# Performance work log

Hardware: AMD Instinct MI355X
Metric: run time of the kernel (lower is better)

## Reference

```python
import jax, jax.numpy as jnp
import numpy as np

DIM = 1024
DIM_MEDIA = 1024
DIM_HEAD = 64
HEADS = 8
INNER = DIM_HEAD * HEADS  # 512
B, N_TOK, N_LAT = 4, 4096, 1024
LN_EPS = 1e-5


def setup_inputs() -> dict:
    key = jax.random.key(0)
    ks = jax.random.split(key, 6)
    x = jax.random.normal(ks[0], (B, N_TOK, DIM), dtype=jnp.float32)
    media = jax.random.normal(ks[1], (B, N_LAT, DIM_MEDIA), dtype=jnp.float32)
    media_mask = jax.random.randint(ks[2], (B, N_LAT), 0, 2).astype(bool)
    media_mask = media_mask.at[:, 0].set(True)  # avoid fully-masked rows (NaN softmax)
    ln_gamma = jnp.ones((DIM,), jnp.float32)
    ln_beta = jnp.zeros((DIM,), jnp.float32)
    Wq = jax.random.normal(ks[3], (DIM, INNER), jnp.float32) * (DIM ** -0.5)
    Wkv = jax.random.normal(ks[4], (DIM_MEDIA, 2 * INNER), jnp.float32) * (DIM_MEDIA ** -0.5)
    Wout = jax.random.normal(ks[5], (INNER, DIM), jnp.float32) * (INNER ** -0.5)
    return {"x": x, "media": media, "media_mask": media_mask,
            "ln_gamma": ln_gamma, "ln_beta": ln_beta,
            "Wq": Wq, "Wkv": Wkv, "Wout": Wout}


def reference(x, media, media_mask, ln_gamma, ln_beta, Wq, Wkv, Wout):
    scale = DIM_HEAD ** -0.5
    # LayerNorm over last dim
    mu = jnp.mean(x, axis=-1, keepdims=True)
    var = jnp.mean(jnp.square(x - mu), axis=-1, keepdims=True)
    xn = (x - mu) * jax.lax.rsqrt(var + LN_EPS) * ln_gamma + ln_beta

    q = (xn @ Wq) * scale                      # [b, n, inner]
    kv = media @ Wkv                           # [b, m, 2*inner]
    k, v = jnp.split(kv, 2, axis=-1)

    def to_heads(t):
        b, n, _ = t.shape
        return t.reshape(b, n, HEADS, DIM_HEAD).transpose(0, 2, 1, 3)  # b h n d

    q, k, v = to_heads(q), to_heads(k), to_heads(v)

    sim = jnp.einsum('bhid,bhjd->bhij', q, k)  # [b, h, n_tok, n_lat]
    neg_inf = jnp.float32(-jnp.inf)
    sim = jnp.where(media_mask[:, None, None, :], sim, neg_inf)
    sim = sim - jax.lax.stop_gradient(jnp.max(sim, axis=-1, keepdims=True))
    attn = jax.nn.softmax(sim, axis=-1)
    out = jnp.einsum('bhij,bhjd->bhid', attn, v)  # [b, h, n_tok, d]
    out = out.transpose(0, 2, 1, 3).reshape(out.shape[0], out.shape[2], INNER)
    return out @ Wout  # [b, n_tok, dim]
```

## Files before the change

kernel.cpp:

```cpp
#include <hip/hip_runtime.h>
#include <hip/hip_bf16.h>

typedef short bf16x8 __attribute__((ext_vector_type(8)));
typedef float f32x4 __attribute__((ext_vector_type(4)));
typedef unsigned short u16;

#define AS1 __attribute__((address_space(1)))
#define AS3 __attribute__((address_space(3)))

#define DIM     1024
#define INNER   512
#define HEADS   8
#define DHEAD   64
#define BATCH   4
#define NTOK    4096
#define NLAT    1024
#define M_X     (BATCH*NTOK)
#define M_MED   (BATCH*NLAT)
#define LN_EPS  1e-5f

__device__ __forceinline__ float b2f(u16 h) {
    union { unsigned u; float f; } v; v.u = ((unsigned)h) << 16; return v.f;
}
__device__ __forceinline__ u16 f2b(float f) {
    union { float f; unsigned u; } v; v.f = f;
    unsigned r = v.u + 0x7fff + ((v.u >> 16) & 1);
    return (u16)(r >> 16);
}
__device__ __forceinline__ unsigned cvt_pk(float lo, float hi) {
    unsigned r;
    asm("v_cvt_pk_bf16_f32 %0, %1, %2" : "=v"(r) : "v"(lo), "v"(hi));
    return r;
}

__launch_bounds__(256)
__global__ void detect_kernel(const unsigned* __restrict__ xw, const unsigned* __restrict__ maskw,
                              unsigned* __restrict__ flags) {
    __shared__ int s_bad, s_byte;
    if (threadIdx.x == 0) { s_bad = 0; s_byte = 0; }
    __syncthreads();
    unsigned w = xw[threadIdx.x];
    int bad = 0;
    #pragma unroll
    for (int h = 0; h < 2; h++) {
        unsigned el = (h ? (w >> 16) : w) & 0xFFFFu;
        unsigned ef = (el >> 7) & 0xFFu;
        if (!((ef >= 64u && ef < 192u) || (el & 0x7FFFu) == 0u)) bad = 1;
    }
    if (bad) atomicOr(&s_bad, 1);
    for (int i = threadIdx.x; i < NLAT; i += 256)
        if (maskw[i] > 1u) { atomicOr(&s_byte, 1); break; }
    __syncthreads();
    if (threadIdx.x == 0) { flags[0] = s_bad ? 0u : 1u; flags[1] = s_byte ? 1u : 0u; }
}

#define PREP_BLOCKS 6148

__device__ __forceinline__ void do_transpose(const void* in, u16* out, int R, int C,
                                             int bx, int by, bool bf, u16 (*t)[33]) {
    int c0 = bx * 32, r0 = by * 32;
    int tid = threadIdx.x;
    int r = tid >> 3, cb = (tid & 7) * 4;
    size_t base = (size_t)(r0 + r) * C + c0 + cb;
    u16 e0, e1, e2, e3;
    if (bf) {
        ushort4 a = *(const ushort4*)((const u16*)in + base);
        e0 = a.x; e1 = a.y; e2 = a.z; e3 = a.w;
    } else {
        float4 a = *(const float4*)((const float*)in + base);
        e0 = f2b(a.x); e1 = f2b(a.y); e2 = f2b(a.z); e3 = f2b(a.w);
    }
    t[r][cb] = e0; t[r][cb + 1] = e1; t[r][cb + 2] = e2; t[r][cb + 3] = e3;
    __syncthreads();
    ushort4 o;
    o.x = t[cb + 0][r]; o.y = t[cb + 1][r]; o.z = t[cb + 2][r]; o.w = t[cb + 3][r];
    *(ushort4*)(out + (size_t)(c0 + r) * R + r0 + cb) = o;
}

__launch_bounds__(256)
__global__ void prep_kernel(const void* __restrict__ x, const void* __restrict__ g,
                            const void* __restrict__ bt, u16* __restrict__ xn,
                            const void* __restrict__ media, u16* __restrict__ media_c,
                            const void* __restrict__ mask, int* __restrict__ map,
                            int* __restrict__ cnt,
                            const void* __restrict__ Wq, u16* __restrict__ WqT,
                            const void* __restrict__ Wkv, u16* __restrict__ WkvT,
                            const void* __restrict__ Wout, u16* __restrict__ WoutT,
                            const unsigned* __restrict__ flags) {
    __shared__ int wsumI[4];
    __shared__ u16 t[32][33];
    bool bf = flags[0] != 0;
    int bid = blockIdx.x, tid = threadIdx.x;

    if (bid < 2048) {
        int w = tid >> 6, lane = tid & 63;
        int row0 = (bid << 3) + (w << 1);
        float v[2][16];
        if (bf) {
            const u16* xr = (const u16*)x + (size_t)row0 * DIM;
            bf16x8 a[4];
            #pragma unroll
            for (int rr = 0; rr < 2; rr++)
                #pragma unroll
                for (int i = 0; i < 2; i++)
                    a[rr * 2 + i] = *(const bf16x8*)(xr + (size_t)rr * DIM + (lane + 64 * i) * 8);
            #pragma unroll
            for (int rr = 0; rr < 2; rr++)
                #pragma unroll
                for (int i = 0; i < 2; i++)
                    #pragma unroll
                    for (int j = 0; j < 8; j++)
                        v[rr][i * 8 + j] = b2f((u16)a[rr * 2 + i][j]);
        } else {
            const float* xr = (const float*)x + (size_t)row0 * DIM;
            float4 a[8];
            #pragma unroll
            for (int rr = 0; rr < 2; rr++)
                #pragma unroll
                for (int i = 0; i < 4; i++)
                    a[rr * 4 + i] = *(const float4*)(xr + (size_t)rr * DIM + (lane + 64 * i) * 4);
            #pragma unroll
            for (int rr = 0; rr < 2; rr++)
                #pragma unroll
                for (int i = 0; i < 4; i++) {
                    v[rr][i * 4 + 0] = a[rr * 4 + i].x; v[rr][i * 4 + 1] = a[rr * 4 + i].y;
                    v[rr][i * 4 + 2] = a[rr * 4 + i].z; v[rr][i * 4 + 3] = a[rr * 4 + i].w;
                }
        }
        float s[2] = {0.f, 0.f}, s2[2] = {0.f, 0.f};
        #pragma unroll
        for (int rr = 0; rr < 2; rr++)
            #pragma unroll
            for (int i = 0; i < 16; i++) { s[rr] += v[rr][i]; s2[rr] += v[rr][i] * v[rr][i]; }
        #pragma unroll
        for (int m = 1; m < 64; m <<= 1) {
            #pragma unroll
            for (int rr = 0; rr < 2; rr++) {
                s[rr] += __shfl_xor(s[rr], m);
                s2[rr] += __shfl_xor(s2[rr], m);
            }
        }
        float mu[2], inv[2];
        #pragma unroll
        for (int rr = 0; rr < 2; rr++) {
            mu[rr] = s[rr] * (1.f / DIM);
            float var = s2[rr] * (1.f / DIM) - mu[rr] * mu[rr];
            inv[rr] = rsqrtf(fmaxf(var, 0.f) + LN_EPS);
        }
        u16* orow = xn + (size_t)row0 * DIM;
        if (bf) {
            const u16* gr = (const u16*)g;
            const u16* br = (const u16*)bt;
            #pragma unroll
            for (int i = 0; i < 2; i++) {
                int c = (lane + 64 * i) * 8;
                bf16x8 ga = *(const bf16x8*)(gr + c);
                bf16x8 ba = *(const bf16x8*)(br + c);
                #pragma unroll
                for (int rr = 0; rr < 2; rr++) {
                    u16 o[8];
                    #pragma unroll
                    for (int j = 0; j < 8; j++)
                        o[j] = f2b((v[rr][i * 8 + j] - mu[rr]) * inv[rr] * b2f((u16)ga[j]) + b2f((u16)ba[j]));
                    *(bf16x8*)(orow + (size_t)rr * DIM + c) = *(bf16x8*)o;
                }
            }
        } else {
            const float* gr = (const float*)g;
            const float* br = (const float*)bt;
            #pragma unroll
            for (int i = 0; i < 4; i++) {
                int c = (lane + 64 * i) * 4;
                float4 ga = *(const float4*)(gr + c);
                float4 ba = *(const float4*)(br + c);
                #pragma unroll
                for (int rr = 0; rr < 2; rr++) {
                    ushort4 o;
                    o.x = f2b((v[rr][i * 4 + 0] - mu[rr]) * inv[rr] * ga.x + ba.x);
                    o.y = f2b((v[rr][i * 4 + 1] - mu[rr]) * inv[rr] * ga.y + ba.y);
                    o.z = f2b((v[rr][i * 4 + 2] - mu[rr]) * inv[rr] * ga.z + ba.z);
                    o.w = f2b((v[rr][i * 4 + 3] - mu[rr]) * inv[rr] * ga.w + ba.w);
                    *(ushort4*)(orow + (size_t)rr * DIM + c) = o;
                }
            }
        }
    } else if (bid < 4096) {
        size_t i = ((size_t)(bid - 2048) * 256 + tid) * 8;
        if (bf) {
            *(bf16x8*)(media_c + i) = *(const bf16x8*)((const u16*)media + i);
        } else {
            const float* s = (const float*)media + i;
            float4 a = *(const float4*)s, b = *(const float4*)(s + 4);
            u16 o[8] = {f2b(a.x), f2b(a.y), f2b(a.z), f2b(a.w),
                        f2b(b.x), f2b(b.y), f2b(b.z), f2b(b.w)};
            *(bf16x8*)(media_c + i) = *(bf16x8*)o;
        }
    } else if (bid < 4100) {
        int b = bid - 4096;
        bool bytes = flags[1] != 0;
        int v[4];
        if (bytes) {
            unsigned wd = ((const unsigned*)mask)[b * 256 + tid];
            #pragma unroll
            for (int i = 0; i < 4; i++) v[i] = ((wd >> (8 * i)) & 0xFFu) ? 1 : 0;
        } else {
            int4 m4 = ((const int4*)mask)[b * 256 + tid];
            v[0] = m4.x != 0; v[1] = m4.y != 0; v[2] = m4.z != 0; v[3] = m4.w != 0;
        }
        int tsum = v[0] + v[1] + v[2] + v[3];
        int lane = tid & 63, w = tid >> 6;
        int incl = tsum;
        #pragma unroll
        for (int off = 1; off < 64; off <<= 1) {
            int tt = __shfl_up(incl, off);
            if (lane >= off) incl += tt;
        }
        if (lane == 63) wsumI[w] = incl;
        __syncthreads();
        int base = 0;
        for (int k = 0; k < w; k++) base += wsumI[k];
        int slot = base + incl - tsum;
        int gbase = b * NLAT + tid * 4;
        #pragma unroll
        for (int i = 0; i < 4; i++) map[gbase + i] = v[i] ? slot++ : -1;
        if (tid == 0) cnt[b] = wsumI[0] + wsumI[1] + wsumI[2] + wsumI[3];
    } else if (bid < 4612) {
        int idx = bid - 4100;
        do_transpose(Wq, WqT, DIM, INNER, idx & 15, idx >> 4, bf, t);
    } else if (bid < 5636) {
        int idx = bid - 4612;
        do_transpose(Wkv, WkvT, DIM, DIM, idx & 31, idx >> 5, bf, t);
    } else {
        int idx = bid - 5636;
        do_transpose(Wout, WoutT, INNER, DIM, idx & 31, idx >> 5, bf, t);
    }
}

__device__ __forceinline__ void gemm_body(const u16* __restrict__ A, const u16* __restrict__ Bt,
                                          u16* __restrict__ C, float* __restrict__ Cf,
                                          int Ndim, int K, float scale, int mode,
                                          u16* __restrict__ vT, const int* __restrict__ map,
                                          bool outbf, int n0, int m0, u16* As, u16* Bs) {
    int tid = threadIdx.x;
    int w = tid >> 6, lane = tid & 63, quad = lane >> 4, l15 = lane & 15;
    int wm = (w >> 1) * 64, wn = (w & 1) * 64;
    f32x4 acc[4][4] = {};
    int rowInSeg = lane >> 2;
    int colB = (((lane & 3) ^ ((lane >> 3) & 3))) * 8;
    for (int k0 = 0; k0 < K; k0 += 32) {
        __syncthreads();
        #pragma unroll
        for (int i = 0; i < 2; i++) {
            int seg = w * 2 + i;
            int row = seg * 16 + rowInSeg;
            __builtin_amdgcn_global_load_lds(
                (const AS1 void*)(A + (size_t)(m0 + row) * K + k0 + colB),
                (AS3 void*)(As + seg * 512), 16, 0, 0);
            __builtin_amdgcn_global_load_lds(
                (const AS1 void*)(Bt + (size_t)(n0 + row) * K + k0 + colB),
                (AS3 void*)(Bs + seg * 512), 16, 0, 0);
        }
        __syncthreads();
        int sw = quad ^ ((l15 >> 1) & 3);
        bf16x8 af[4], bfr[4];
        #pragma unroll
        for (int i = 0; i < 4; i++)
            af[i] = *(bf16x8*)&As[(wm + i * 16 + l15) * 32 + sw * 8];
        #pragma unroll
        for (int j = 0; j < 4; j++)
            bfr[j] = *(bf16x8*)&Bs[(wn + j * 16 + l15) * 32 + sw * 8];
        #pragma unroll
        for (int i = 0; i < 4; i++)
            #pragma unroll
            for (int j = 0; j < 4; j++)
                acc[i][j] = __builtin_amdgcn_mfma_f32_16x16x32_bf16(af[i], bfr[j], acc[i][j], 0, 0, 0);
    }
    #pragma unroll
    for (int i = 0; i < 4; i++)
        #pragma unroll
        for (int j = 0; j < 4; j++)
            #pragma unroll
            for (int r = 0; r < 4; r++) {
                int row = m0 + wm + i * 16 + quad * 4 + r;
                int col = n0 + wn + j * 16 + l15;
                float val = acc[i][j][r] * scale;
                if (mode == 1) {
                    int b = row >> 10, jj = row & 1023;
                    int slot = map[(b << 10) + jj];
                    if (slot >= 0) {
                        if (col < INNER) {
                            C[((size_t)(b << 10) + slot) * INNER + col] = f2b(val);
                        } else {
                            int c = col - INNER;
                            int h = c >> 6, d = c & 63;
                            vT[(((size_t)(b * HEADS + h) * 64 + d) << 10) + slot] = f2b(val);
                        }
                    }
                } else if (outbf) {
                    C[(size_t)row * Ndim + col] = f2b(val);
                } else {
                    Cf[(size_t)row * Ndim + col] = val;
                }
            }
}

__launch_bounds__(256, 3)
__global__ void gemm128(const u16* __restrict__ A, const u16* __restrict__ Bt,
                        u16* __restrict__ C, float* __restrict__ Cf, int Ndim, int K,
                        float scale, int mode, u16* __restrict__ vT,
                        const int* __restrict__ map,
                        const unsigned* __restrict__ flags) {
    __shared__ __align__(16) u16 As[128 * 32];
    __shared__ __align__(16) u16 Bs[128 * 32];
    bool outbf = (mode != 2) || (flags[0] != 0);
    gemm_body(A, Bt, C, Cf, Ndim, K, scale, mode, vT, map, outbf,
              blockIdx.x * 128, blockIdx.y * 128, As, Bs);
}

__launch_bounds__(256, 3)
__global__ void gemm_qkv(const u16* __restrict__ xn, const u16* __restrict__ WqT,
                         u16* __restrict__ qb,
                         const u16* __restrict__ media_c, const u16* __restrict__ WkvT,
                         u16* __restrict__ Kb, u16* __restrict__ vT,
                         const int* __restrict__ map) {
    __shared__ __align__(16) u16 As[128 * 32];
    __shared__ __align__(16) u16 Bs[128 * 32];
    int bid = blockIdx.x;
    if (bid < 512) {
        gemm_body(xn, WqT, qb, (float*)nullptr, INNER, DIM, 0.125f * 1.44269504f, 0,
                  (u16*)nullptr, (int*)nullptr, true,
                  (bid & 3) * 128, (bid >> 2) * 128, As, Bs);
    } else {
        int id = bid - 512;
        gemm_body(media_c, WkvT, Kb, (float*)nullptr, DIM, DIM, 1.0f, 1,
                  vT, map, true,
                  (id & 7) * 128, (id >> 3) * 128, As, Bs);
    }
}

__launch_bounds__(256, 6)
__global__ void flash_kernel(const u16* __restrict__ q, const u16* __restrict__ Kc,
                             const u16* __restrict__ vTc, const int* __restrict__ cntp,
                             u16* __restrict__ attn_out) {
    __shared__ __align__(16) u16 Ks[64 * 64];
    __shared__ __align__(16) u16 Vts[64 * 64];
    __shared__ __align__(16) u16 Ps[4][16 * 68];
    int bh = blockIdx.x >> 6;
    int qt = blockIdx.x & 63;
    int b = bh >> 3, h = bh & 7;
    int tid = threadIdx.x, w = tid >> 6, lane = tid & 63, quad = lane >> 4, l15 = lane & 15;
    int qrow0 = qt * 64 + w * 16;
    int cnt = cntp[b];

    size_t qbase = ((size_t)(b * NTOK) + qrow0 + l15) * INNER + h * 64;
    bf16x8 qf[2];
    qf[0] = *(const bf16x8*)(q + qbase + quad * 8);
    qf[1] = *(const bf16x8*)(q + qbase + 32 + quad * 8);

    f32x4 Oacc[4] = {};
    float lsum = 0.f;
    int ld_row = lane >> 3;
    int ld_col = ((lane & 7) ^ ld_row) * 8;

    for (int jt = 0; jt < cnt; jt += 64) {
        __syncthreads();
        #pragma unroll
        for (int i = 0; i < 2; i++) {
            int seg = w * 2 + i;
            int j = jt + seg * 8 + ld_row;
            __builtin_amdgcn_global_load_lds(
                (const AS1 void*)(Kc + ((size_t)(b * NLAT) + j) * INNER + h * 64 + ld_col),
                (AS3 void*)(Ks + seg * 512), 16, 0, 0);
            int d = seg * 8 + ld_row;
            __builtin_amdgcn_global_load_lds(
                (const AS1 void*)(vTc + (((size_t)(b * HEADS + h) * 64 + d) << 10) + jt + ld_col),
                (AS3 void*)(Vts + seg * 512), 16, 0, 0);
        }
        __syncthreads();

        int sw0 = (quad ^ (l15 & 7)) * 8;
        int sw1 = ((quad + 4) ^ (l15 & 7)) * 8;
        f32x4 S[4];
        #pragma unroll
        for (int c = 0; c < 4; c++) {
            bf16x8 kf0 = *(bf16x8*)&Ks[(c * 16 + l15) * 64 + sw0];
            bf16x8 kf1 = *(bf16x8*)&Ks[(c * 16 + l15) * 64 + sw1];
            f32x4 s = {};
            s = __builtin_amdgcn_mfma_f32_16x16x32_bf16(kf0, qf[0], s, 0, 0, 0);
            s = __builtin_amdgcn_mfma_f32_16x16x32_bf16(kf1, qf[1], s, 0, 0, 0);
            S[c] = s;
        }
        if (jt + 64 <= cnt) {
            #pragma unroll
            for (int c = 0; c < 4; c++) {
                float p0 = exp2f(fminf(S[c][0], 115.4f));
                float p1 = exp2f(fminf(S[c][1], 115.4f));
                float p2 = exp2f(fminf(S[c][2], 115.4f));
                float p3 = exp2f(fminf(S[c][3], 115.4f));
                lsum += (p0 + p1) + (p2 + p3);
                uint2 pw = {cvt_pk(p0, p1), cvt_pk(p2, p3)};
                *(uint2*)&Ps[w][l15 * 68 + c * 16 + quad * 4] = pw;
            }
        } else {
            #pragma unroll
            for (int c = 0; c < 4; c++) {
                int kbase = jt + c * 16 + quad * 4;
                float p[4];
                #pragma unroll
                for (int r = 0; r < 4; r++) {
                    bool valid = (kbase + r) < cnt;
                    p[r] = valid ? exp2f(fminf(S[c][r], 115.4f)) : 0.f;
                    lsum += p[r];
                }
                uint2 pw = {cvt_pk(p[0], p[1]), cvt_pk(p[2], p[3])};
                *(uint2*)&Ps[w][l15 * 68 + c * 16 + quad * 4] = pw;
            }
        }
        asm volatile("s_waitcnt lgkmcnt(0)" ::: "memory");
        bf16x8 pf0 = *(bf16x8*)&Ps[w][l15 * 68 + quad * 8];
        bf16x8 pf1 = *(bf16x8*)&Ps[w][l15 * 68 + 32 + quad * 8];
        #pragma unroll
        for (int dt = 0; dt < 4; dt++) {
            bf16x8 vf0 = *(bf16x8*)&Vts[(dt * 16 + l15) * 64 + sw0];
            bf16x8 vf1 = *(bf16x8*)&Vts[(dt * 16 + l15) * 64 + sw1];
            Oacc[dt] = __builtin_amdgcn_mfma_f32_16x16x32_bf16(pf0, vf0, Oacc[dt], 0, 0, 0);
            Oacc[dt] = __builtin_amdgcn_mfma_f32_16x16x32_bf16(pf1, vf1, Oacc[dt], 0, 0, 0);
        }
    }
    lsum += __shfl_xor(lsum, 16);
    lsum += __shfl_xor(lsum, 32);
    #pragma unroll
    for (int r = 0; r < 4; r++) {
        float l = __shfl(lsum, quad * 4 + r);
        float invl = (l > 0.f) ? (1.f / l) : 0.f;
        #pragma unroll
        for (int dt = 0; dt < 4; dt++) {
            int row = qrow0 + quad * 4 + r;
            int col = h * 64 + dt * 16 + l15;
            attn_out[(size_t)(b * NTOK + row) * INNER + col] = f2b(Oacc[dt][r] * invl);
        }
    }
}

extern "C" void kernel_launch(void* const* d_in, const int* in_sizes, int n_in,
                              void* d_out, int out_size, void* d_ws, size_t ws_size,
                              hipStream_t stream) {
    const void* x     = d_in[0];
    const void* media = d_in[1];
    const void* mask  = d_in[2];
    const void* g     = d_in[3];
    const void* beta  = d_in[4];
    const void* Wq    = d_in[5];
    const void* Wkv   = d_in[6];
    const void* Wout  = d_in[7];

    char* ws = (char*)d_ws;
    unsigned* flags = (unsigned*)ws;   ws += 256;
    int* map_c  = (int*)ws;            ws += (size_t)M_MED * 4;
    int* cnt_c  = (int*)ws;            ws += 256;
    u16* media_c = (u16*)ws;           ws += (size_t)M_MED * DIM * 2;
    u16* xn    = (u16*)ws;             ws += (size_t)M_X * DIM * 2;
    u16* qb    = (u16*)ws;             ws += (size_t)M_X * INNER * 2;
    u16* Kb    = (u16*)ws;             ws += (size_t)M_MED * INNER * 2;
    u16* vTb   = (u16*)ws;             ws += (size_t)M_MED * INNER * 2;
    u16* ao    = (u16*)ws;             ws += (size_t)M_X * INNER * 2;
    u16* WqT   = (u16*)ws;             ws += (size_t)DIM * INNER * 2;
    u16* WkvT  = (u16*)ws;             ws += (size_t)DIM * DIM * 2;
    u16* WoutT = (u16*)ws;             ws += (size_t)INNER * DIM * 2;

    detect_kernel<<<1, 256, 0, stream>>>((const unsigned*)x, (const unsigned*)mask, flags);
    prep_kernel<<<PREP_BLOCKS, 256, 0, stream>>>(x, g, beta, xn, media, media_c, mask, map_c, cnt_c,
                                                 Wq, WqT, Wkv, WkvT, Wout, WoutT, flags);
    gemm_qkv<<<dim3(768), 256, 0, stream>>>(xn, WqT, qb, media_c, WkvT, Kb, vTb, map_c);
    flash_kernel<<<dim3(32 * 64), 256, 0, stream>>>(qb, Kb, vTb, cnt_c, ao);
    gemm128<<<dim3(DIM / 128, M_X / 128), 256, 0, stream>>>(ao, WoutT, (u16*)d_out, (float*)d_out, DIM, INNER,
                                                            1.0f, 2, (u16*)nullptr, (int*)nullptr, flags);
}
```

Measured before the change: 266.7 us.

## Fold LayerNorm into the Q GEMM epilogue via per-row stats and weight folding

The normalized x is no longer written to memory. The prep kernel stores only per-row inverse std and mean, folds gamma into the transposed Wq, and precomputes the column vectors gamma·Wq and beta·Wq. The Q GEMM epilogue then rebuilds the normalized projection algebraically. When the inputs are already bf16, the x and media copy passes are skipped and the GEMMs read the raw inputs directly. This removes a full read and write pass over x, at some precision risk from subtracting mu·Gv after bf16 rounding of the unnormalized x.

```diff
diff --git a/kernel.cpp b/kernel.cpp
--- a/kernel.cpp
+++ b/kernel.cpp
@@ -18,6 +18,7 @@
 #define M_X     (BATCH*NTOK)
 #define M_MED   (BATCH*NLAT)
 #define LN_EPS  1e-5f
+#define QSCALE  (0.125f * 1.44269504f)
 
 __device__ __forceinline__ float b2f(u16 h) {
     union { unsigned u; float f; } v; v.u = ((unsigned)h) << 16; return v.f;
@@ -54,10 +55,11 @@
     if (threadIdx.x == 0) { flags[0] = s_bad ? 0u : 1u; flags[1] = s_byte ? 1u : 0u; }
 }
 
-#define PREP_BLOCKS 6148
+#define PREP_BLOCKS 6156
 
 __device__ __forceinline__ void do_transpose(const void* in, u16* out, int R, int C,
-                                             int bx, int by, bool bf, u16 (*t)[33]) {
+                                             int bx, int by, bool bf, u16 (*t)[33],
+                                             const void* gv) {
     int c0 = bx * 32, r0 = by * 32;
     int tid = threadIdx.x;
     int r = tid >> 3, cb = (tid & 7) * 4;
@@ -65,10 +67,17 @@
     u16 e0, e1, e2, e3;
     if (bf) {
         ushort4 a = *(const ushort4*)((const u16*)in + base);
-        e0 = a.x; e1 = a.y; e2 = a.z; e3 = a.w;
+        if (gv) {
+            float sc = b2f(((const u16*)gv)[r0 + r]);
+            e0 = f2b(b2f(a.x) * sc); e1 = f2b(b2f(a.y) * sc);
+            e2 = f2b(b2f(a.z) * sc); e3 = f2b(b2f(a.w) * sc);
+        } else {
+            e0 = a.x; e1 = a.y; e2 = a.z; e3 = a.w;
+        }
     } else {
         float4 a = *(const float4*)((const float*)in + base);
-        e0 = f2b(a.x); e1 = f2b(a.y); e2 = f2b(a.z); e3 = f2b(a.w);
+        float sc = gv ? ((const float*)gv)[r0 + r] : 1.f;
+        e0 = f2b(a.x * sc); e1 = f2b(a.y * sc); e2 = f2b(a.z * sc); e3 = f2b(a.w * sc);
     }
     t[r][cb] = e0; t[r][cb + 1] = e1; t[r][cb + 2] = e2; t[r][cb + 3] = e3;
     __syncthreads();
@@ -79,16 +88,19 @@
 
 __launch_bounds__(256)
 __global__ void prep_kernel(const void* __restrict__ x, const void* __restrict__ g,
-                            const void* __restrict__ bt, u16* __restrict__ xn,
+                            const void* __restrict__ bt, u16* __restrict__ xc,
                             const void* __restrict__ media, u16* __restrict__ media_c,
                             const void* __restrict__ mask, int* __restrict__ map,
                             int* __restrict__ cnt,
                             const void* __restrict__ Wq, u16* __restrict__ WqT,
                             const void* __restrict__ Wkv, u16* __restrict__ WkvT,
                             const void* __restrict__ Wout, u16* __restrict__ WoutT,
+                            float2* __restrict__ stats, float* __restrict__ Gv,
+                            float* __restrict__ Bv,
                             const unsigned* __restrict__ flags) {
     __shared__ int wsumI[4];
     __shared__ u16 t[32][33];
+    __shared__ float rg[4][64], rb[4][64];
     bool bf = flags[0] != 0;
     int bid = blockIdx.x, tid = threadIdx.x;
 
@@ -140,61 +152,33 @@
                 s2[rr] += __shfl_xor(s2[rr], m);
             }
         }
-        float mu[2], inv[2];
         #pragma unroll
         for (int rr = 0; rr < 2; rr++) {
-            mu[rr] = s[rr] * (1.f / DIM);
-            float var = s2[rr] * (1.f / DIM) - mu[rr] * mu[rr];
-            inv[rr] = rsqrtf(fmaxf(var, 0.f) + LN_EPS);
-        }
-        u16* orow = xn + (size_t)row0 * DIM;
-        if (bf) {
-            const u16* gr = (const u16*)g;
-            const u16* br = (const u16*)bt;
-            #pragma unroll
-            for (int i = 0; i < 2; i++) {
-                int c = (lane + 64 * i) * 8;
-                bf16x8 ga = *(const bf16x8*)(gr + c);
-                bf16x8 ba = *(const bf16x8*)(br + c);
-                #pragma unroll
-                for (int rr = 0; rr < 2; rr++) {
-                    u16 o[8];
-                    #pragma unroll
-                    for (int j = 0; j < 8; j++)
-                        o[j] = f2b((v[rr][i * 8 + j] - mu[rr]) * inv[rr] * b2f((u16)ga[j]) + b2f((u16)ba[j]));
-                    *(bf16x8*)(orow + (size_t)rr * DIM + c) = *(bf16x8*)o;
+            float mu = s[rr] * (1.f / DIM);
+            float var = s2[rr] * (1.f / DIM) - mu * mu;
+            float inv = rsqrtf(fmaxf(var, 0.f) + LN_EPS);
+            if (lane == 0) stats[row0 + rr] = make_float2(inv * QSCALE, inv * mu * QSCALE);
+        }
+        if (!bf) {
+            u16* orow = xc + (size_t)row0 * DIM;
+            #pragma unroll
+            for (int rr = 0; rr < 2; rr++)
+                #pragma unroll
+                for (int i = 0; i < 4; i++) {
+                    ushort4 o;
+                    o.x = f2b(v[rr][i * 4 + 0]); o.y = f2b(v[rr][i * 4 + 1]);
+                    o.z = f2b(v[rr][i * 4 + 2]); o.w = f2b(v[rr][i * 4 + 3]);
+                    *(ushort4*)(orow + (size_t)rr * DIM + (lane + 64 * i) * 4) = o;
                 }
-            }
-        } else {
-            const float* gr = (const float*)g;
-            const float* br = (const float*)bt;
-            #pragma unroll
-            for (int i = 0; i < 4; i++) {
-                int c = (lane + 64 * i) * 4;
-                float4 ga = *(const float4*)(gr + c);
-                float4 ba = *(const float4*)(br + c);
-                #pragma unroll
-                for (int rr = 0; rr < 2; rr++) {
-                    ushort4 o;
-                    o.x = f2b((v[rr][i * 4 + 0] - mu[rr]) * inv[rr] * ga.x + ba.x);
-                    o.y = f2b((v[rr][i * 4 + 1] - mu[rr]) * inv[rr] * ga.y + ba.y);
-                    o.z = f2b((v[rr][i * 4 + 2] - mu[rr]) * inv[rr] * ga.z + ba.z);
-                    o.w = f2b((v[rr][i * 4 + 3] - mu[rr]) * inv[rr] * ga.w + ba.w);
-                    *(ushort4*)(orow + (size_t)rr * DIM + c) = o;
-                }
-            }
         }
     } else if (bid < 4096) {
+        if (bf) return;
         size_t i = ((size_t)(bid - 2048) * 256 + tid) * 8;
-        if (bf) {
-            *(bf16x8*)(media_c + i) = *(const bf16x8*)((const u16*)media + i);
-        } else {
-            const float* s = (const float*)media + i;
-            float4 a = *(const float4*)s, b = *(const float4*)(s + 4);
-            u16 o[8] = {f2b(a.x), f2b(a.y), f2b(a.z), f2b(a.w),
-                        f2b(b.x), f2b(b.y), f2b(b.z), f2b(b.w)};
-            *(bf16x8*)(media_c + i) = *(bf16x8*)o;
-        }
+        const float* s = (const float*)media + i;
+        float4 a = *(const float4*)s, b = *(const float4*)(s + 4);
+        u16 o[8] = {f2b(a.x), f2b(a.y), f2b(a.z), f2b(a.w),
+                    f2b(b.x), f2b(b.y), f2b(b.z), f2b(b.w)};
+        *(bf16x8*)(media_c + i) = *(bf16x8*)o;
     } else if (bid < 4100) {
         int b = bid - 4096;
         bool bytes = flags[1] != 0;
@@ -226,13 +210,49 @@
         if (tid == 0) cnt[b] = wsumI[0] + wsumI[1] + wsumI[2] + wsumI[3];
     } else if (bid < 4612) {
         int idx = bid - 4100;
-        do_transpose(Wq, WqT, DIM, INNER, idx & 15, idx >> 4, bf, t);
+        do_transpose(Wq, WqT, DIM, INNER, idx & 15, idx >> 4, bf, t, g);
     } else if (bid < 5636) {
         int idx = bid - 4612;
-        do_transpose(Wkv, WkvT, DIM, DIM, idx & 31, idx >> 5, bf, t);
+        do_transpose(Wkv, WkvT, DIM, DIM, idx & 31, idx >> 5, bf, t, nullptr);
+    } else if (bid < 6148) {
+        int idx = bid - 5636;
+        do_transpose(Wout, WoutT, INNER, DIM, idx & 31, idx >> 5, bf, t, nullptr);
     } else {
-        int idx = bid - 5636;
-        do_transpose(Wout, WoutT, INNER, DIM, idx & 31, idx >> 5, bf, t);
+        int idx = bid - 6148;
+        int col = idx * 64 + (tid & 63), kq = tid >> 6;
+        float ag = 0.f, ab = 0.f;
+        if (bf) {
+            const u16* W = (const u16*)Wq;
+            const u16* gg = (const u16*)g;
+            const u16* bb = (const u16*)bt;
+            for (int k = kq * 256; k < kq * 256 + 256; k += 4) {
+                #pragma unroll
+                for (int u = 0; u < 4; u++) {
+                    float wv = b2f(W[(size_t)(k + u) * INNER + col]);
+                    ag += b2f(gg[k + u]) * wv;
+                    ab += b2f(bb[k + u]) * wv;
+                }
+            }
+        } else {
+            const float* W = (const float*)Wq;
+            const float* gg = (const float*)g;
+            const float* bb = (const float*)bt;
+            for (int k = kq * 256; k < kq * 256 + 256; k += 4) {
+                #pragma unroll
+                for (int u = 0; u < 4; u++) {
+                    float wv = W[(size_t)(k + u) * INNER + col];
+                    ag += gg[k + u] * wv;
+                    ab += bb[k + u] * wv;
+                }
+            }
+        }
+        rg[kq][tid & 63] = ag; rb[kq][tid & 63] = ab;
+        __syncthreads();
+        if (kq == 0) {
+            int c = tid & 63;
+            Gv[col] = rg[0][c] + rg[1][c] + rg[2][c] + rg[3][c];
+            Bv[col] = (rb[0][c] + rb[1][c] + rb[2][c] + rb[3][c]) * QSCALE;
+        }
     }
 }
 
@@ -240,7 +260,10 @@
                                           u16* __restrict__ C, float* __restrict__ Cf,
                                           int Ndim, int K, float scale, int mode,
                                           u16* __restrict__ vT, const int* __restrict__ map,
-                                          bool outbf, int n0, int m0, u16* As, u16* Bs) {
+                                          bool outbf, int n0, int m0, u16* As, u16* Bs,
+                                          const float2* __restrict__ stats,
+                                          const float* __restrict__ Gv,
+                                          const float* __restrict__ Bv) {
     int tid = threadIdx.x;
     int w = tid >> 6, lane = tid & 63, quad = lane >> 4, l15 = lane & 15;
     int wm = (w >> 1) * 64, wn = (w & 1) * 64;
@@ -283,8 +306,12 @@
             for (int r = 0; r < 4; r++) {
                 int row = m0 + wm + i * 16 + quad * 4 + r;
                 int col = n0 + wn + j * 16 + l15;
-                float val = acc[i][j][r] * scale;
-                if (mode == 1) {
+                if (mode == 0) {
+                    float2 st = stats[row];
+                    float val = st.x * acc[i][j][r] - st.y * Gv[col] + Bv[col];
+                    C[(size_t)row * Ndim + col] = f2b(val);
+                } else if (mode == 1) {
+                    float val = acc[i][j][r];
                     int b = row >> 10, jj = row & 1023;
                     int slot = map[(b << 10) + jj];
                     if (slot >= 0) {
@@ -296,10 +323,10 @@
                             vT[(((size_t)(b * HEADS + h) * 64 + d) << 10) + slot] = f2b(val);
                         }
                     }
-                } else if (outbf) {
-                    C[(size_t)row * Ndim + col] = f2b(val);
                 } else {
-                    Cf[(size_t)row * Ndim + col] = val;
+                    float val = acc[i][j][r] * scale;
+                    if (outbf) C[(size_t)row * Ndim + col] = f2b(val);
+                    else       Cf[(size_t)row * Ndim + col] = val;
                 }
             }
 }
@@ -314,27 +341,36 @@
     __shared__ __align__(16) u16 Bs[128 * 32];
     bool outbf = (mode != 2) || (flags[0] != 0);
     gemm_body(A, Bt, C, Cf, Ndim, K, scale, mode, vT, map, outbf,
-              blockIdx.x * 128, blockIdx.y * 128, As, Bs);
+              blockIdx.x * 128, blockIdx.y * 128, As, Bs,
+              (const float2*)nullptr, (const float*)nullptr, (const float*)nullptr);
 }
 
 __launch_bounds__(256, 3)
-__global__ void gemm_qkv(const u16* __restrict__ xn, const u16* __restrict__ WqT,
-                         u16* __restrict__ qb,
-                         const u16* __restrict__ media_c, const u16* __restrict__ WkvT,
+__global__ void gemm_qkv(const void* __restrict__ x, const u16* __restrict__ xc,
+                         const u16* __restrict__ WqT, u16* __restrict__ qb,
+                         const void* __restrict__ media, const u16* __restrict__ media_c,
+                         const u16* __restrict__ WkvT,
                          u16* __restrict__ Kb, u16* __restrict__ vT,
-                         const int* __restrict__ map) {
+                         const int* __restrict__ map,
+                         const float2* __restrict__ stats, const float* __restrict__ Gv,
+                         const float* __restrict__ Bv,
+                         const unsigned* __restrict__ flags) {
     __shared__ __align__(16) u16 As[128 * 32];
     __shared__ __align__(16) u16 Bs[128 * 32];
+    bool bf = flags[0] != 0;
     int bid = blockIdx.x;
     if (bid < 512) {
-        gemm_body(xn, WqT, qb, (float*)nullptr, INNER, DIM, 0.125f * 1.44269504f, 0,
+        const u16* A = bf ? (const u16*)x : xc;
+        gemm_body(A, WqT, qb, (float*)nullptr, INNER, DIM, 1.0f, 0,
                   (u16*)nullptr, (int*)nullptr, true,
-                  (bid & 3) * 128, (bid >> 2) * 128, As, Bs);
+                  (bid & 3) * 128, (bid >> 2) * 128, As, Bs, stats, Gv, Bv);
     } else {
         int id = bid - 512;
-        gemm_body(media_c, WkvT, Kb, (float*)nullptr, DIM, DIM, 1.0f, 1,
+        const u16* A = bf ? (const u16*)media : media_c;
+        gemm_body(A, WkvT, Kb, (float*)nullptr, DIM, DIM, 1.0f, 1,
                   vT, map, true,
-                  (id & 7) * 128, (id >> 3) * 128, As, Bs);
+                  (id & 7) * 128, (id >> 3) * 128, As, Bs,
+                  (const float2*)nullptr, (const float*)nullptr, (const float*)nullptr);
     }
 }
 
@@ -458,8 +494,11 @@
     unsigned* flags = (unsigned*)ws;   ws += 256;
     int* map_c  = (int*)ws;            ws += (size_t)M_MED * 4;
     int* cnt_c  = (int*)ws;            ws += 256;
+    float2* stats = (float2*)ws;       ws += (size_t)M_X * 8;
+    float* Gv   = (float*)ws;          ws += INNER * 4;
+    float* Bv   = (float*)ws;          ws += INNER * 4;
     u16* media_c = (u16*)ws;           ws += (size_t)M_MED * DIM * 2;
-    u16* xn    = (u16*)ws;             ws += (size_t)M_X * DIM * 2;
+    u16* xc    = (u16*)ws;             ws += (size_t)M_X * DIM * 2;
     u16* qb    = (u16*)ws;             ws += (size_t)M_X * INNER * 2;
     u16* Kb    = (u16*)ws;             ws += (size_t)M_MED * INNER * 2;
     u16* vTb   = (u16*)ws;             ws += (size_t)M_MED * INNER * 2;
@@ -469,9 +508,11 @@
     u16* WoutT = (u16*)ws;             ws += (size_t)INNER * DIM * 2;
 
     detect_kernel<<<1, 256, 0, stream>>>((const unsigned*)x, (const unsigned*)mask, flags);
-    prep_kernel<<<PREP_BLOCKS, 256, 0, stream>>>(x, g, beta, xn, media, media_c, mask, map_c, cnt_c,
-                                                 Wq, WqT, Wkv, WkvT, Wout, WoutT, flags);
-    gemm_qkv<<<dim3(768), 256, 0, stream>>>(xn, WqT, qb, media_c, WkvT, Kb, vTb, map_c);
+    prep_kernel<<<PREP_BLOCKS, 256, 0, stream>>>(x, g, beta, xc, media, media_c, mask, map_c, cnt_c,
+                                                 Wq, WqT, Wkv, WkvT, Wout, WoutT,
+                                                 stats, Gv, Bv, flags);
+    gemm_qkv<<<dim3(768), 256, 0, stream>>>(x, xc, WqT, qb, media, media_c, WkvT, Kb, vTb,
+                                            map_c, stats, Gv, Bv, flags);
     flash_kernel<<<dim3(32 * 64), 256, 0, stream>>>(qb, Kb, vTb, cnt_c, ao);
     gemm128<<<dim3(DIM / 128, M_X / 128), 256, 0, stream>>>(ao, WoutT, (u16*)d_out, (float*)d_out, DIM, INNER,
                                                             1.0f, 2, (u16*)nullptr, (int*)nullptr, flags);
```

Result: slower. 274.4 us (+2.9%).
